# Optimization experiments

Measured on AMD Instinct MI355X. Metric: run time of the kernel, lower is better.

The kernel has to match this reference:

```python
import jax, jax.numpy as jnp
import numpy as np

GRID_SIZE = 5
SPLINE_ORDER = 3
GRID_RANGE = (-1.0, 1.0)
EPS = 1e-8


def _make_grid():
    h = (GRID_RANGE[1] - GRID_RANGE[0]) / GRID_SIZE
    # knots: [-spline_order, ..., grid_size + spline_order] * h + lo  -> 12 values
    return jnp.arange(-SPLINE_ORDER, GRID_SIZE + SPLINE_ORDER + 1, dtype=jnp.float32) * h + GRID_RANGE[0]


def _bspline_basis(x, grid):
    # x: [N, in]  ->  bases: [N, in, num_basis] with num_basis = grid_size + spline_order
    xe = x[..., None]                                   # [N, in, 1]
    bases = ((xe >= grid[:-1]) & (xe < grid[1:])).astype(x.dtype)  # [N, in, 11]
    for k in range(1, SPLINE_ORDER + 1):
        left = (xe - grid[: -(k + 1)]) / (grid[k:-1] - grid[: -(k + 1)] + EPS) * bases[..., :-1]
        right = (grid[k + 1:] - xe) / (grid[k + 1:] - grid[1:-k] + EPS) * bases[..., 1:]
        bases = left + right
    return bases                                        # [N, in, 8]


def setup_inputs() -> dict:
    key = jax.random.key(0)
    k1, k2, k3 = jax.random.split(key, 3)
    in_f, out_f, num_basis = 1024, 1024, GRID_SIZE + SPLINE_ORDER
    N = 4096
    x = jax.random.normal(k1, (N, in_f), dtype=jnp.float32)
    base_weight = jax.random.normal(k2, (out_f, in_f), dtype=jnp.float32) * (1.0 / np.sqrt(in_f))
    base_bias = jnp.zeros((out_f,), dtype=jnp.float32)
    spline_weight = jax.random.normal(k3, (out_f, in_f, num_basis), dtype=jnp.float32) * (1.0 / np.sqrt(in_f))
    return {"x": x, "base_weight": base_weight, "base_bias": base_bias, "spline_weight": spline_weight}


def reference(x, base_weight, base_bias, spline_weight):
    grid = _make_grid()
    # base path: SiLU(x) @ W_base^T + b
    base_out = jax.nn.silu(x) @ base_weight.T + base_bias          # [N, out]
    # spline path: Cox-de Boor basis then contraction over (in, basis)
    basis = _bspline_basis(x, grid)                                 # [N, in, 8]
    spline_out = jnp.einsum('nib,oib->no', basis, spline_weight)    # [N, out]
    return base_out + spline_out
```

## Files before the change

kernel.cpp:

```cpp
#include <hip/hip_runtime.h>
#include <hip/hip_bf16.h>
#include <stdint.h>

#define IN_F 1024
#define OUT_F 1024
#define NB 8
#define KDIM (IN_F + IN_F * NB)
#define NROWS 4096
#define SLICE_ELEMS (NROWS * OUT_F)
#define PREP_BLOCKS ((NROWS * IN_F) / 256)
#define WCONV_BLOCKS ((OUT_F * KDIM) / (4 * 256))

typedef __attribute__((ext_vector_type(8))) short bf16x8;
typedef __attribute__((ext_vector_type(4))) short bf16x4;
typedef __attribute__((ext_vector_type(4))) float f32x4;

__device__ __forceinline__ void bspline8(float x, float b8[8]) {
  float u = (x + 2.2f) * 2.5f;
  bool in = (u >= 0.0f) && (u < 11.0f);
  float uc = fminf(fmaxf(u, 0.0f), 10.99f);
  int i = (int)uc;
  float f = uc - (float)i;
  float g = 1.0f - f;
  float f2 = f * f, f3 = f2 * f;
  const float s = 1.0f / 6.0f;
  float v0 = f3 * s;
  float v1 = (-3.0f * f3 + 3.0f * f2 + 3.0f * f + 1.0f) * s;
  float v2 = (3.0f * f3 - 6.0f * f2 + 4.0f) * s;
  float v3 = g * g * g * s;
#pragma unroll
  for (int j = 0; j < 8; ++j) {
    int d = i - j;
    float r = (d == 0) ? v0 : (d == 1) ? v1 : (d == 2) ? v2 : (d == 3) ? v3 : 0.0f;
    b8[j] = in ? r : 0.0f;
  }
}

__global__ void prep_all_kernel(const float* __restrict__ x, const float* __restrict__ bw,
                                const float* __restrict__ sw, __hip_bfloat16* __restrict__ A,
                                __hip_bfloat16* __restrict__ W) {
  if (blockIdx.x < PREP_BLOCKS) {
    int idx = blockIdx.x * 256 + threadIdx.x;
    int n = idx >> 10;
    int i = idx & 1023;
    float xv = x[idx];
    float sl = xv / (1.0f + __expf(-xv));
    __hip_bfloat16* row = A + (size_t)n * KDIM;
    row[i] = __float2bfloat16(sl);
    float b8[8];
    bspline8(xv, b8);
    alignas(16) __hip_bfloat16 tmp[8];
#pragma unroll
    for (int c = 0; c < 8; ++c) tmp[c] = __float2bfloat16(b8[c]);
    *(bf16x8*)(row + IN_F + i * 8) = *(const bf16x8*)tmp;
  } else {
    int v = (blockIdx.x - PREP_BLOCKS) * 256 + threadIdx.x;
    int e = v * 4;
    int o = e / KDIM;
    int k = e - o * KDIM;
    float4 val = (k < IN_F) ? *(const float4*)(bw + o * IN_F + k)
                            : *(const float4*)(sw + (size_t)o * (IN_F * NB) + (k - IN_F));
    alignas(8) __hip_bfloat16 t[4];
    t[0] = __float2bfloat16(val.x);
    t[1] = __float2bfloat16(val.y);
    t[2] = __float2bfloat16(val.z);
    t[3] = __float2bfloat16(val.w);
    *(bf16x4*)(W + e) = *(const bf16x4*)t;
  }
}

__global__ __launch_bounds__(256) void gemm_kernel(const __hip_bfloat16* __restrict__ A,
                                                   const __hip_bfloat16* __restrict__ W,
                                                   float* __restrict__ dst,
                                                   const float* __restrict__ bias,
                                                   int kslice, int use_bias) {
  __shared__ __hip_bfloat16 lA[2][128 * 32];
  __shared__ __hip_bfloat16 lB[2][128 * 32];
  const int tid = threadIdx.x;
  const int wave = tid >> 6;
  const int lane = tid & 63;
  const int bm = blockIdx.x * 128;
  const int bn = blockIdx.y * 128;
  const int z = blockIdx.z;
  float* __restrict__ d = dst + (size_t)z * SLICE_ELEMS;
  const int kbeg = z * kslice;
  const int iters = kslice / 32;
  const int srow = lane & 15;
  const int skc = (lane >> 4) * 8;
  const int wm = (wave & 1) * 64;
  const int wn = (wave >> 1) * 64;
  const int r = lane & 15;
  const int quad = lane >> 4;

  const int g0 = wave * 2;
  const __hip_bfloat16* gA0 = A + (size_t)(bm + g0 * 16 + srow) * KDIM + kbeg + skc;
  const __hip_bfloat16* gA1 = gA0 + (size_t)16 * KDIM;
  const __hip_bfloat16* gB0 = W + (size_t)(bn + g0 * 16 + srow) * KDIM + kbeg + skc;
  const __hip_bfloat16* gB1 = gB0 + (size_t)16 * KDIM;
  const int o0 = g0 * 512;
  const int o1 = o0 + 512;

  f32x4 acc[4][4];
#pragma unroll
  for (int a = 0; a < 4; ++a)
#pragma unroll
    for (int b = 0; b < 4; ++b) acc[a][b] = (f32x4){0.f, 0.f, 0.f, 0.f};

#define STAGE(IT, BUF)                                                                          \
  do {                                                                                          \
    const int koff = (IT)*32;                                                                   \
    __builtin_amdgcn_global_load_lds((const __attribute__((address_space(1))) void*)(gA0 + koff), \
                                     (__attribute__((address_space(3))) void*)(lA[BUF] + o0), 16, \
                                     0, 0);                                                     \
    __builtin_amdgcn_global_load_lds((const __attribute__((address_space(1))) void*)(gA1 + koff), \
                                     (__attribute__((address_space(3))) void*)(lA[BUF] + o1), 16, \
                                     0, 0);                                                     \
    __builtin_amdgcn_global_load_lds((const __attribute__((address_space(1))) void*)(gB0 + koff), \
                                     (__attribute__((address_space(3))) void*)(lB[BUF] + o0), 16, \
                                     0, 0);                                                     \
    __builtin_amdgcn_global_load_lds((const __attribute__((address_space(1))) void*)(gB1 + koff), \
                                     (__attribute__((address_space(3))) void*)(lB[BUF] + o1), 16, \
                                     0, 0);                                                     \
  } while (0)

  STAGE(0, 0);
  __syncthreads();

  for (int it = 0; it < iters; ++it) {
    const int p = it & 1;
    if (it + 1 < iters) STAGE(it + 1, p ^ 1);

    bf16x8 af[4], bfr[4];
#pragma unroll
    for (int t = 0; t < 4; ++t) {
      af[t] = *(const bf16x8*)(lA[p] + ((wm >> 4) + t) * 512 + lane * 8);
      bfr[t] = *(const bf16x8*)(lB[p] + ((wn >> 4) + t) * 512 + lane * 8);
    }
#pragma unroll
    for (int tm = 0; tm < 4; ++tm)
#pragma unroll
      for (int tn = 0; tn < 4; ++tn)
        acc[tm][tn] =
            __builtin_amdgcn_mfma_f32_16x16x32_bf16(af[tm], bfr[tn], acc[tm][tn], 0, 0, 0);

    __syncthreads();
  }
#undef STAGE

#pragma unroll
  for (int tm = 0; tm < 4; ++tm) {
#pragma unroll
    for (int tn = 0; tn < 4; ++tn) {
      const int col = bn + wn + tn * 16 + r;
      const float bv = use_bias ? bias[col] : 0.0f;
#pragma unroll
      for (int reg = 0; reg < 4; ++reg) {
        const int rowi = bm + wm + tm * 16 + quad * 4 + reg;
        d[(size_t)rowi * OUT_F + col] = acc[tm][tn][reg] + bv;
      }
    }
  }
}

__global__ void reduce_kernel(const float* __restrict__ P, const float* __restrict__ bias,
                              float* __restrict__ out, int S) {
  int v = blockIdx.x * 256 + threadIdx.x;
  int e = v * 4;
  int o = e & (OUT_F - 1);
  float4 acc = *(const float4*)(bias + o);
  for (int s = 0; s < S; ++s) {
    float4 p = *(const float4*)(P + (size_t)s * SLICE_ELEMS + e);
    acc.x += p.x;
    acc.y += p.y;
    acc.z += p.z;
    acc.w += p.w;
  }
  *(float4*)(out + e) = acc;
}

__global__ void kan_fallback(const float* __restrict__ x, const float* __restrict__ bw,
                             const float* __restrict__ bb, const float* __restrict__ sw,
                             float* __restrict__ out) {
  __shared__ float act[KDIM];
  int n = blockIdx.x;
  for (int i = threadIdx.x; i < IN_F; i += 256) {
    float xv = x[(size_t)n * IN_F + i];
    act[i] = xv / (1.0f + __expf(-xv));
    float b8[8];
    bspline8(xv, b8);
#pragma unroll
    for (int c = 0; c < 8; ++c) act[IN_F + i * 8 + c] = b8[c];
  }
  __syncthreads();
  for (int o = threadIdx.x; o < OUT_F; o += 256) {
    float s = bb[o];
    const float* wbp = bw + (size_t)o * IN_F;
    for (int k = 0; k < IN_F; ++k) s += act[k] * wbp[k];
    const float* wsp = sw + (size_t)o * (IN_F * NB);
    for (int k = 0; k < IN_F * NB; ++k) s += act[IN_F + k] * wsp[k];
    out[(size_t)n * OUT_F + o] = s;
  }
}

extern "C" void kernel_launch(void* const* d_in, const int* in_sizes, int n_in, void* d_out,
                              int out_size, void* d_ws, size_t ws_size, hipStream_t stream) {
  const float* x = (const float*)d_in[0];
  const float* bw = (const float*)d_in[1];
  const float* bb = (const float*)d_in[2];
  const float* sw = (const float*)d_in[3];
  float* out = (float*)d_out;

  const size_t needA = (size_t)NROWS * KDIM * 2;
  const size_t needW = (size_t)OUT_F * KDIM * 2;
  const size_t sliceB = (size_t)SLICE_ELEMS * 4;
  if (ws_size < needA + needW) {
    kan_fallback<<<NROWS, 256, 0, stream>>>(x, bw, bb, sw, out);
    return;
  }
  __hip_bfloat16* A = (__hip_bfloat16*)d_ws;
  __hip_bfloat16* W = (__hip_bfloat16*)((char*)d_ws + needA);
  float* P = (float*)((char*)d_ws + needA + needW);
  const size_t avail = ws_size - needA - needW;
  int S = (avail >= 2 * sliceB) ? 2 : 1;

  prep_all_kernel<<<PREP_BLOCKS + WCONV_BLOCKS, 256, 0, stream>>>(x, bw, sw, A, W);
  if (S == 1) {
    gemm_kernel<<<dim3(NROWS / 128, OUT_F / 128, 1), 256, 0, stream>>>(A, W, out, bb, KDIM, 1);
  } else {
    gemm_kernel<<<dim3(NROWS / 128, OUT_F / 128, S), 256, 0, stream>>>(A, W, P, bb, KDIM / S, 0);
    reduce_kernel<<<SLICE_ELEMS / (4 * 256), 256, 0, stream>>>(P, bb, out, S);
  }
}
```

Baseline: 263.1 us.

## Replace split-K partial buffers and reduce kernel with atomic accumulation into output

The output is initialised with the bias inside the prep kernel. The GEMM now splits K four ways and each slice atomically adds its tile into the output, so the partial-sum workspace and the separate reduce kernel are gone. Launch bounds are raised to request four blocks per CU. This removes a kernel launch and the partial-buffer write/read traffic and adds K-parallelism, in exchange for contended float atomics (four per output element) and results that vary slightly between runs.

After: 292.6 us. 1.11x slower.

```diff
diff --git a/kernel.cpp b/kernel.cpp
--- a/kernel.cpp
+++ b/kernel.cpp
@@ -8,8 +8,11 @@
 #define KDIM (IN_F + IN_F * NB)
 #define NROWS 4096
 #define SLICE_ELEMS (NROWS * OUT_F)
+#define INIT_BLOCKS (SLICE_ELEMS / (4 * 256))
 #define PREP_BLOCKS ((NROWS * IN_F) / 256)
 #define WCONV_BLOCKS ((OUT_F * KDIM) / (4 * 256))
+#define SPLIT 4
+#define KSLICE (KDIM / SPLIT)
 
 typedef __attribute__((ext_vector_type(8))) short bf16x8;
 typedef __attribute__((ext_vector_type(4))) short bf16x4;
@@ -37,10 +40,16 @@
 }
 
 __global__ void prep_all_kernel(const float* __restrict__ x, const float* __restrict__ bw,
-                                const float* __restrict__ sw, __hip_bfloat16* __restrict__ A,
-                                __hip_bfloat16* __restrict__ W) {
-  if (blockIdx.x < PREP_BLOCKS) {
-    int idx = blockIdx.x * 256 + threadIdx.x;
+                                const float* __restrict__ sw, const float* __restrict__ bb,
+                                __hip_bfloat16* __restrict__ A, __hip_bfloat16* __restrict__ W,
+                                float* __restrict__ out) {
+  if (blockIdx.x < INIT_BLOCKS) {
+    int v = blockIdx.x * 256 + threadIdx.x;
+    int e = v * 4;
+    int o = e & (OUT_F - 1);
+    *(float4*)(out + e) = *(const float4*)(bb + o);
+  } else if (blockIdx.x < INIT_BLOCKS + PREP_BLOCKS) {
+    int idx = (blockIdx.x - INIT_BLOCKS) * 256 + threadIdx.x;
     int n = idx >> 10;
     int i = idx & 1023;
     float xv = x[idx];
@@ -54,7 +63,7 @@
     for (int c = 0; c < 8; ++c) tmp[c] = __float2bfloat16(b8[c]);
     *(bf16x8*)(row + IN_F + i * 8) = *(const bf16x8*)tmp;
   } else {
-    int v = (blockIdx.x - PREP_BLOCKS) * 256 + threadIdx.x;
+    int v = (blockIdx.x - INIT_BLOCKS - PREP_BLOCKS) * 256 + threadIdx.x;
     int e = v * 4;
     int o = e / KDIM;
     int k = e - o * KDIM;
@@ -69,11 +78,9 @@
   }
 }
 
-__global__ __launch_bounds__(256) void gemm_kernel(const __hip_bfloat16* __restrict__ A,
-                                                   const __hip_bfloat16* __restrict__ W,
-                                                   float* __restrict__ dst,
-                                                   const float* __restrict__ bias,
-                                                   int kslice, int use_bias) {
+__global__ __launch_bounds__(256, 4) void gemm_kernel(const __hip_bfloat16* __restrict__ A,
+                                                      const __hip_bfloat16* __restrict__ W,
+                                                      float* __restrict__ out) {
   __shared__ __hip_bfloat16 lA[2][128 * 32];
   __shared__ __hip_bfloat16 lB[2][128 * 32];
   const int tid = threadIdx.x;
@@ -81,10 +88,8 @@
   const int lane = tid & 63;
   const int bm = blockIdx.x * 128;
   const int bn = blockIdx.y * 128;
-  const int z = blockIdx.z;
-  float* __restrict__ d = dst + (size_t)z * SLICE_ELEMS;
-  const int kbeg = z * kslice;
-  const int iters = kslice / 32;
+  const int kbeg = blockIdx.z * KSLICE;
+  const int iters = KSLICE / 32;
   const int srow = lane & 15;
   const int skc = (lane >> 4) * 8;
   const int wm = (wave & 1) * 64;
@@ -106,21 +111,21 @@
 #pragma unroll
     for (int b = 0; b < 4; ++b) acc[a][b] = (f32x4){0.f, 0.f, 0.f, 0.f};
 
-#define STAGE(IT, BUF)                                                                          \
-  do {                                                                                          \
-    const int koff = (IT)*32;                                                                   \
+#define STAGE(IT, BUF)                                                                            \
+  do {                                                                                            \
+    const int koff = (IT)*32;                                                                     \
     __builtin_amdgcn_global_load_lds((const __attribute__((address_space(1))) void*)(gA0 + koff), \
                                      (__attribute__((address_space(3))) void*)(lA[BUF] + o0), 16, \
-                                     0, 0);                                                     \
+                                     0, 0);                                                       \
     __builtin_amdgcn_global_load_lds((const __attribute__((address_space(1))) void*)(gA1 + koff), \
                                      (__attribute__((address_space(3))) void*)(lA[BUF] + o1), 16, \
-                                     0, 0);                                                     \
+                                     0, 0);                                                       \
     __builtin_amdgcn_global_load_lds((const __attribute__((address_space(1))) void*)(gB0 + koff), \
                                      (__attribute__((address_space(3))) void*)(lB[BUF] + o0), 16, \
-                                     0, 0);                                                     \
+                                     0, 0);                                                       \
     __builtin_amdgcn_global_load_lds((const __attribute__((address_space(1))) void*)(gB1 + koff), \
                                      (__attribute__((address_space(3))) void*)(lB[BUF] + o1), 16, \
-                                     0, 0);                                                     \
+                                     0, 0);                                                       \
   } while (0)
 
   STAGE(0, 0);
@@ -133,8 +138,8 @@
     bf16x8 af[4], bfr[4];
 #pragma unroll
     for (int t = 0; t < 4; ++t) {
-      af[t] = *(const bf16x8*)(lA[p] + ((wm >> 4) + t) * 512 + lane * 8);
-      bfr[t] = *(const bf16x8*)(lB[p] + ((wn >> 4) + t) * 512 + lane * 8);
+      af[t] = *(const bf16x8*)&lA[p][((wm >> 4) + t) * 512 + lane * 8];
+      bfr[t] = *(const bf16x8*)&lB[p][((wn >> 4) + t) * 512 + lane * 8];
     }
 #pragma unroll
     for (int tm = 0; tm < 4; ++tm)
@@ -152,30 +157,13 @@
 #pragma unroll
     for (int tn = 0; tn < 4; ++tn) {
       const int col = bn + wn + tn * 16 + r;
-      const float bv = use_bias ? bias[col] : 0.0f;
 #pragma unroll
       for (int reg = 0; reg < 4; ++reg) {
         const int rowi = bm + wm + tm * 16 + quad * 4 + reg;
-        d[(size_t)rowi * OUT_F + col] = acc[tm][tn][reg] + bv;
+        atomicAdd(out + (size_t)rowi * OUT_F + col, acc[tm][tn][reg]);
       }
     }
   }
-}
-
-__global__ void reduce_kernel(const float* __restrict__ P, const float* __restrict__ bias,
-                              float* __restrict__ out, int S) {
-  int v = blockIdx.x * 256 + threadIdx.x;
-  int e = v * 4;
-  int o = e & (OUT_F - 1);
-  float4 acc = *(const float4*)(bias + o);
-  for (int s = 0; s < S; ++s) {
-    float4 p = *(const float4*)(P + (size_t)s * SLICE_ELEMS + e);
-    acc.x += p.x;
-    acc.y += p.y;
-    acc.z += p.z;
-    acc.w += p.w;
-  }
-  *(float4*)(out + e) = acc;
 }
 
 __global__ void kan_fallback(const float* __restrict__ x, const float* __restrict__ bw,
@@ -212,22 +200,14 @@
 
   const size_t needA = (size_t)NROWS * KDIM * 2;
   const size_t needW = (size_t)OUT_F * KDIM * 2;
-  const size_t sliceB = (size_t)SLICE_ELEMS * 4;
   if (ws_size < needA + needW) {
     kan_fallback<<<NROWS, 256, 0, stream>>>(x, bw, bb, sw, out);
     return;
   }
   __hip_bfloat16* A = (__hip_bfloat16*)d_ws;
   __hip_bfloat16* W = (__hip_bfloat16*)((char*)d_ws + needA);
-  float* P = (float*)((char*)d_ws + needA + needW);
-  const size_t avail = ws_size - needA - needW;
-  int S = (avail >= 2 * sliceB) ? 2 : 1;
-
-  prep_all_kernel<<<PREP_BLOCKS + WCONV_BLOCKS, 256, 0, stream>>>(x, bw, sw, A, W);
-  if (S == 1) {
-    gemm_kernel<<<dim3(NROWS / 128, OUT_F / 128, 1), 256, 0, stream>>>(A, W, out, bb, KDIM, 1);
-  } else {
-    gemm_kernel<<<dim3(NROWS / 128, OUT_F / 128, S), 256, 0, stream>>>(A, W, P, bb, KDIM / S, 0);
-    reduce_kernel<<<SLICE_ELEMS / (4 * 256), 256, 0, stream>>>(P, bb, out, S);
-  }
-}
+
+  prep_all_kernel<<<INIT_BLOCKS + PREP_BLOCKS + WCONV_BLOCKS, 256, 0, stream>>>(x, bw, sw, bb, A,
+                                                                                W, out);
+  gemm_kernel<<<dim3(NROWS / 128, OUT_F / 128, SPLIT), 256, 0, stream>>>(A, W, out);
+}
```
